# Optimization experiments

Hardware: AMD Instinct MI355X
Metric: run time of the kernel (lower is better)

The kernel has to match this reference:

```python
import jax, jax.numpy as jnp
import numpy as np

# Dims: B=batch, S=seq, H=hidden, I=intermediate, E=experts, K=top-k
B, S, H, I, E, K = 1, 1024, 1024, 1024, 8, 2


def setup_inputs() -> dict:
    key = jax.random.key(0)
    k0, k1, k2, k3 = jax.random.split(key, 4)
    return {
        "hidden_states": jax.random.normal(k0, (B, S, H), dtype=jnp.float32),
        "router_weight": jax.random.normal(k1, (E, H), dtype=jnp.float32) * 0.02,
        "gate_up_proj": jax.random.normal(k2, (E, H, 2 * I), dtype=jnp.float32) * 0.02,
        "gate_up_proj_bias": jnp.zeros((E, 2 * I), dtype=jnp.float32),
        "down_proj": jax.random.normal(k3, (E, I, H), dtype=jnp.float32) * 0.02,
        "down_proj_bias": jnp.zeros((E, H), dtype=jnp.float32),
    }


def reference(hidden_states, router_weight, gate_up_proj, gate_up_proj_bias,
              down_proj, down_proj_bias):
    b, s, h = hidden_states.shape
    flat = hidden_states.reshape(b * s, h)            # [N, H]
    n = flat.shape[0]

    # Router: softmax over experts, then top-k selection
    logits = flat @ router_weight.T                   # [N, E]
    scores = jax.nn.softmax(logits, axis=-1)          # [N, E]
    _, indices = jax.lax.top_k(scores, K)             # [N, K]

    # Dense all-experts GEMM (matches original: every token through every expert)
    gate_up = jnp.einsum('nh,eho->neo', flat, gate_up_proj) + gate_up_proj_bias  # [N, E, 2I]
    gate = jnp.minimum(gate_up[..., ::2], 7.0)        # interleaved gate, clamp max
    up = jnp.clip(gate_up[..., 1::2], -7.0, 7.0)      # interleaved up, clamp both
    activated = (up + 1.0) * gate * jax.nn.sigmoid(gate * 1.702)  # [N, E, I]

    expert_out = jnp.einsum('nei,eih->neh', activated, down_proj) + down_proj_bias  # [N, E, H]

    # Masked combine: zero weights except at top-k experts
    top_w = jnp.take_along_axis(scores, indices, axis=-1)                     # [N, K]
    weights = jnp.zeros_like(scores).at[jnp.arange(n)[:, None], indices].set(top_w)  # [N, E]
    out = (expert_out * weights[..., None]).sum(axis=1)                       # [N, H]
    return out.reshape(b, s, h), scores
```

## Files before the change

### kernel.cpp

```cpp
#include <hip/hip_runtime.h>
#include <hip/hip_bf16.h>

typedef __attribute__((ext_vector_type(8))) short short8;
typedef __attribute__((ext_vector_type(4))) float f32x4;

#define NTOK 1024
#define HDIM 1024
#define IDIM 1024
#define NEXP 8
#define NCOL 2048

#define WS_COUNTS   0
#define WS_Q        960
#define WS_LTOK     1024
#define WS_LW       (WS_LTOK + NEXP*NTOK*4)
#define WS_XBF      131072
#define WS_ACT      (WS_XBF + NTOK*HDIM*2)
#define WS_W1B      (WS_ACT + 2*NTOK*IDIM*2)
#define WS_W2B      (WS_W1B + (size_t)NEXP*NCOL*HDIM*2)

static __device__ __forceinline__ unsigned short f2bf(float x) {
    __hip_bfloat16 h = __float2bfloat16(x);
    return __builtin_bit_cast(unsigned short, h);
}

#define GLDS16(g, l) __builtin_amdgcn_global_load_lds( \
    (const __attribute__((address_space(1))) void*)(g), \
    (__attribute__((address_space(3))) void*)(l), 16, 0, 0)

static __device__ __forceinline__ float4 xpose4(float4 v, int i) {
    float x = (i & 1) ? v.x : v.y;
    float y = (i & 1) ? v.z : v.w;
    x = __shfl_xor(x, 1); y = __shfl_xor(y, 1);
    if (i & 1) { v.x = x; v.z = y; } else { v.y = x; v.w = y; }
    float x2 = (i & 2) ? v.x : v.z;
    float y2 = (i & 2) ? v.y : v.w;
    x2 = __shfl_xor(x2, 2); y2 = __shfl_xor(y2, 2);
    if (i & 2) { v.x = x2; v.y = y2; } else { v.z = x2; v.w = y2; }
    return v;
}

__global__ __launch_bounds__(256) void prep_kernel(
    const float* __restrict__ flat, const float* __restrict__ rw,
    const float* __restrict__ gup,
    float* __restrict__ scores, int* __restrict__ counts,
    int* __restrict__ ltok, float* __restrict__ lw,
    unsigned short* __restrict__ xbf, unsigned short* __restrict__ w1b)
{
    __shared__ unsigned short tile[64][70];
    const int b = blockIdx.x;
    const int t = threadIdx.x;

    if (b >= 256) {
        const int tid = b - 256;
        const int e = tid >> 9, rem = tid & 511, kb = rem >> 5, cb = rem & 31;
        const int i4 = t & 3, g = t >> 2;
        const int rq = g >> 4, cq = (g & 15) * 4;
        const float* s0 = gup + ((size_t)e * 1024 + kb * 64 + rq * 16 + i4) * NCOL
                         + cb * 64 + cq;
        float4 vr[4];
#pragma unroll
        for (int it = 0; it < 4; ++it)
            vr[it] = *(const float4*)(s0 + (size_t)(it * 4) * NCOL);
        const int c = cq + i4;
#pragma unroll
        for (int it = 0; it < 4; ++it) {
            float4 v = xpose4(vr[it], i4);
            ushort4 o;
            o.x = f2bf(v.x); o.y = f2bf(v.y); o.z = f2bf(v.z); o.w = f2bf(v.w);
            *(ushort4*)&tile[c][rq * 16 + it * 4] = o;
        }
        __syncthreads();
        unsigned short* d0 = w1b + (((size_t)e * 16 + kb) * NCOL + cb * 64) * 64;
#pragma unroll
        for (int p = 0; p < 2; ++p) {
            int cc = p * 32 + (t >> 3), q = t & 7;
            short8 vv = *(const short8*)&tile[cc][q * 8];
            *(short8*)&d0[(size_t)cc * 64 + q * 8] = vv;
        }
        return;
    }

    const int n = b * 4 + (t >> 6);
    const int l = t & 63;
    float acc[NEXP];
#pragma unroll
    for (int e = 0; e < NEXP; ++e) acc[e] = 0.f;
    const float* xrow = flat + (size_t)n * HDIM;
#pragma unroll
    for (int j = 0; j < 4; ++j) {
        int h = j * 256 + l * 4;
        float4 v = *(const float4*)&xrow[h];
        ushort4 xb;
        xb.x = f2bf(v.x); xb.y = f2bf(v.y); xb.z = f2bf(v.z); xb.w = f2bf(v.w);
        *(ushort4*)&xbf[(size_t)n * HDIM + h] = xb;
#pragma unroll
        for (int e = 0; e < NEXP; ++e) {
            float4 wv = *(const float4*)&rw[e * HDIM + h];
            acc[e] += v.x * wv.x + v.y * wv.y + v.z * wv.z + v.w * wv.w;
        }
    }
#pragma unroll
    for (int e = 0; e < NEXP; ++e) {
#pragma unroll
        for (int off = 32; off > 0; off >>= 1)
            acc[e] += __shfl_down(acc[e], off);
    }
    if (l == 0) {
        float m = acc[0];
#pragma unroll
        for (int e = 1; e < NEXP; ++e) m = fmaxf(m, acc[e]);
        float s = 0.f, p[NEXP];
#pragma unroll
        for (int e = 0; e < NEXP; ++e) { p[e] = __expf(acc[e] - m); s += p[e]; }
        float inv = 1.f / s;
#pragma unroll
        for (int e = 0; e < NEXP; ++e) { p[e] *= inv; scores[n * NEXP + e] = p[e]; }
        int i0 = 0;
#pragma unroll
        for (int e = 1; e < NEXP; ++e) if (p[e] > p[i0]) i0 = e;
        int i1 = (i0 == 0) ? 1 : 0;
#pragma unroll
        for (int e = 0; e < NEXP; ++e) if (e != i0 && p[e] > p[i1]) i1 = e;
        int pos0 = atomicAdd(&counts[i0 * 32], 1);
        ltok[i0 * NTOK + pos0] = n; lw[i0 * NTOK + pos0] = p[i0];
        int pos1 = atomicAdd(&counts[i1 * 32], 1);
        ltok[i1 * NTOK + pos1] = n; lw[i1 * NTOK + pos1] = p[i1];
    }
}

__global__ __launch_bounds__(512) void gemm1_kernel(
    const unsigned short* __restrict__ xbf, const unsigned short* __restrict__ w1b,
    const float* __restrict__ gbias,
    const int* __restrict__ counts,
    const int* __restrict__ ltok, unsigned short* __restrict__ act,
    const float* __restrict__ dp, unsigned short* __restrict__ w2b,
    int* __restrict__ tq)
{
    const int e = blockIdx.z;
    int cnt = 0, off = 0;
#pragma unroll
    for (int j2 = 0; j2 < NEXP; ++j2) {
        int c = counts[j2 * 32];
        if (j2 < e) off += c;
        if (j2 == e) cnt = c;
    }
    const int by = blockIdx.y;
    const int bx = blockIdx.x;
    const int t = threadIdx.x;

    __shared__ unsigned short As[2][128][64];
    __shared__ unsigned short Bs[2][128][64];
    __shared__ int toks[128];
    __shared__ int tbase;

    if (by * 128 >= cnt) {
        unsigned short (*ttile)[64][70] = (unsigned short (*)[64][70])(&As[0][0][0]);
        const int half = t >> 8, tt = t & 255;
        const int i4 = tt & 3, g = tt >> 2;
        const int rq = g >> 4, cq = (g & 15) * 4;
        for (;;) {
            if (t == 0) tbase = atomicAdd(tq, 2);
            __syncthreads();
            int base = tbase;
            if (base >= 2048) break;
            int myt = base + half;
            int te = myt >> 8, rem = myt & 255, kb = rem >> 4, cb = rem & 15;
            const float* s0 = dp + ((size_t)te * 1024 + kb * 64 + rq * 16 + i4) * HDIM
                             + cb * 64 + cq;
            float4 vr[4];
#pragma unroll
            for (int it = 0; it < 4; ++it)
                vr[it] = *(const float4*)(s0 + (size_t)(it * 4) * HDIM);
            const int c = cq + i4;
#pragma unroll
            for (int it = 0; it < 4; ++it) {
                float4 v = xpose4(vr[it], i4);
                ushort4 o;
                o.x = f2bf(v.x); o.y = f2bf(v.y); o.z = f2bf(v.z); o.w = f2bf(v.w);
                *(ushort4*)&ttile[half][c][rq * 16 + it * 4] = o;
            }
            __syncthreads();
            unsigned short* d0 = w2b + (((size_t)te * 16 + kb) * HDIM + cb * 64) * 64;
#pragma unroll
            for (int p = 0; p < 2; ++p) {
                int cc = p * 32 + (tt >> 3), q = tt & 7;
                short8 vv = *(const short8*)&ttile[half][cc][q * 8];
                *(short8*)&d0[(size_t)cc * 64 + q * 8] = vv;
            }
        }
        return;
    }

    const int l = t & 63, w = t >> 6;
    const int wm = w >> 2, wn = w & 3;
    if (t < 128) toks[t] = ltok[e * NTOK + min(by * 128 + t, cnt - 1)];
    __syncthreads();

    const int li = l & 7, lr = l >> 3;
    const int kswz = (li ^ lr) * 8;
    const unsigned short* asrc[2];
    const unsigned short* bsrc[2];
#pragma unroll
    for (int j = 0; j < 2; ++j) {
        int rr = (w * 2 + j) * 8 + lr;
        asrc[j] = xbf + (size_t)toks[rr] * HDIM + kswz;
        bsrc[j] = w1b + (size_t)e * 16 * NCOL * 64 + (size_t)(bx * 128 + rr) * 64 + kswz;
    }

    f32x4 acc[4][2];
#pragma unroll
    for (int m = 0; m < 4; ++m)
#pragma unroll
        for (int n = 0; n < 2; ++n) acc[m][n] = 0.f;

#pragma unroll
    for (int j = 0; j < 2; ++j) {
        GLDS16(asrc[j], &As[0][(w * 2 + j) * 8][0]);
        GLDS16(bsrc[j], &Bs[0][(w * 2 + j) * 8][0]);
    }

    const int lg = l >> 4, lo = l & 15;
    const int cq0 = ((0 + lg) ^ (lo & 7)) * 8;
    const int cq1 = ((4 + lg) ^ (lo & 7)) * 8;

    for (int ks = 0; ks < HDIM / 64; ++ks) {
        const int p = ks & 1;
        __builtin_amdgcn_s_barrier();
        if (ks + 1 < HDIM / 64) {
            const int kadvA = (ks + 1) * 64;
            const size_t kadvB = (size_t)(ks + 1) * NCOL * 64;
#pragma unroll
            for (int j = 0; j < 2; ++j) {
                GLDS16(asrc[j] + kadvA, &As[p ^ 1][(w * 2 + j) * 8][0]);
                GLDS16(bsrc[j] + kadvB, &Bs[p ^ 1][(w * 2 + j) * 8][0]);
            }
            asm volatile("s_waitcnt vmcnt(4)" ::: "memory");
        } else {
            asm volatile("s_waitcnt vmcnt(0)" ::: "memory");
        }
        __builtin_amdgcn_sched_barrier(0);
        __builtin_amdgcn_s_barrier();
#pragma unroll
        for (int q = 0; q < 2; ++q) {
            const int cq = q ? cq1 : cq0;
            short8 a0 = *(const short8*)&As[p][wm * 64 +  0 + lo][cq];
            short8 a1 = *(const short8*)&As[p][wm * 64 + 16 + lo][cq];
            short8 a2 = *(const short8*)&As[p][wm * 64 + 32 + lo][cq];
            short8 a3 = *(const short8*)&As[p][wm * 64 + 48 + lo][cq];
            short8 b0 = *(const short8*)&Bs[p][wn * 32 +  0 + lo][cq];
            short8 b1 = *(const short8*)&Bs[p][wn * 32 + 16 + lo][cq];
#pragma unroll
            for (int m = 0; m < 4; ++m) {
                short8 am = (m == 0) ? a0 : (m == 1) ? a1 : (m == 2) ? a2 : a3;
                acc[m][0] = __builtin_amdgcn_mfma_f32_16x16x32_bf16(am, b0, acc[m][0], 0, 0, 0);
                acc[m][1] = __builtin_amdgcn_mfma_f32_16x16x32_bf16(am, b1, acc[m][1], 0, 0, 0);
            }
        }
    }

    const int rj = lg * 4;
#pragma unroll
    for (int m = 0; m < 4; ++m) {
#pragma unroll
        for (int n = 0; n < 2; ++n) {
            int col = bx * 128 + wn * 32 + n * 16 + lo;
            float bias = gbias[e * NCOL + col];
#pragma unroll
            for (int j = 0; j < 4; ++j) {
                int slot = by * 128 + wm * 64 + m * 16 + rj + j;
                float val = acc[m][n][j] + bias;
                float other = __shfl_xor(val, 1);
                float g = (l & 1) ? other : val;
                float u = (l & 1) ? val : other;
                g = fminf(g, 7.f);
                u = fminf(fmaxf(u, -7.f), 7.f);
                float av = (u + 1.f) * g * (1.f / (1.f + __expf(-1.702f * g)));
                if (!(l & 1) && slot < cnt)
                    act[(size_t)(off + slot) * IDIM + (col >> 1)] = f2bf(av);
            }
        }
    }
}

__global__ __launch_bounds__(512) void gemm2_kernel(
    const unsigned short* __restrict__ act, const unsigned short* __restrict__ w2b,
    const float* __restrict__ dbias,
    const int* __restrict__ counts,
    const int* __restrict__ ltok,
    const float* __restrict__ lw, float* __restrict__ outbuf)
{
    const int e = blockIdx.z;
    int cnt = 0, off = 0;
#pragma unroll
    for (int j2 = 0; j2 < NEXP; ++j2) {
        int c = counts[j2 * 32];
        if (j2 < e) off += c;
        if (j2 == e) cnt = c;
    }
    const int by = blockIdx.y;
    if (by * 128 >= cnt) return;
    const int bx = blockIdx.x;
    const int t = threadIdx.x;
    const int l = t & 63, w = t >> 6;
    const int wm = w >> 1, wn = w & 1;

    __shared__ unsigned short As[2][128][64];
    __shared__ unsigned short Bs[2][64][64];
    __shared__ int toks[128];
    __shared__ float wts[128];
    if (t < 128) {
        int cl = min(by * 128 + t, cnt - 1);
        toks[t] = ltok[e * NTOK + cl];
        wts[t]  = lw[e * NTOK + cl];
    }
    __syncthreads();

    const int li = l & 7, lr = l >> 3;
    const int kswz = (li ^ lr) * 8;
    const unsigned short* asrc[2];
#pragma unroll
    for (int j = 0; j < 2; ++j) {
        int rr = (w * 2 + j) * 8 + lr;
        asrc[j] = act + (size_t)(off + min(by * 128 + rr, cnt - 1)) * IDIM + kswz;
    }
    const unsigned short* bsrc = w2b + (size_t)e * 16 * HDIM * 64
                               + (size_t)(bx * 64 + w * 8 + lr) * 64 + kswz;

    f32x4 acc[2][2];
#pragma unroll
    for (int m = 0; m < 2; ++m)
#pragma unroll
        for (int n = 0; n < 2; ++n) acc[m][n] = 0.f;

#pragma unroll
    for (int j = 0; j < 2; ++j)
        GLDS16(asrc[j], &As[0][(w * 2 + j) * 8][0]);
    GLDS16(bsrc, &Bs[0][w * 8][0]);

    const int lg = l >> 4, lo = l & 15;
    const int cq0 = ((0 + lg) ^ (lo & 7)) * 8;
    const int cq1 = ((4 + lg) ^ (lo & 7)) * 8;

    for (int ks = 0; ks < IDIM / 64; ++ks) {
        const int p = ks & 1;
        __builtin_amdgcn_s_barrier();
        if (ks + 1 < IDIM / 64) {
            const int kadvA = (ks + 1) * 64;
            const size_t kadvB = (size_t)(ks + 1) * HDIM * 64;
#pragma unroll
            for (int j = 0; j < 2; ++j)
                GLDS16(asrc[j] + kadvA, &As[p ^ 1][(w * 2 + j) * 8][0]);
            GLDS16(bsrc + kadvB, &Bs[p ^ 1][w * 8][0]);
            asm volatile("s_waitcnt vmcnt(3)" ::: "memory");
        } else {
            asm volatile("s_waitcnt vmcnt(0)" ::: "memory");
        }
        __builtin_amdgcn_sched_barrier(0);
        __builtin_amdgcn_s_barrier();
#pragma unroll
        for (int q = 0; q < 2; ++q) {
            const int cq = q ? cq1 : cq0;
            short8 a0 = *(const short8*)&As[p][wm * 32 +  0 + lo][cq];
            short8 a1 = *(const short8*)&As[p][wm * 32 + 16 + lo][cq];
            short8 b0 = *(const short8*)&Bs[p][wn * 32 +  0 + lo][cq];
            short8 b1 = *(const short8*)&Bs[p][wn * 32 + 16 + lo][cq];
            acc[0][0] = __builtin_amdgcn_mfma_f32_16x16x32_bf16(a0, b0, acc[0][0], 0, 0, 0);
            acc[1][0] = __builtin_amdgcn_mfma_f32_16x16x32_bf16(a1, b0, acc[1][0], 0, 0, 0);
            acc[0][1] = __builtin_amdgcn_mfma_f32_16x16x32_bf16(a0, b1, acc[0][1], 0, 0, 0);
            acc[1][1] = __builtin_amdgcn_mfma_f32_16x16x32_bf16(a1, b1, acc[1][1], 0, 0, 0);
        }
    }

    const int rj = lg * 4;
#pragma unroll
    for (int m = 0; m < 2; ++m) {
#pragma unroll
        for (int n = 0; n < 2; ++n) {
            int col = bx * 64 + wn * 32 + n * 16 + lo;
            float bias = dbias[e * HDIM + col];
#pragma unroll
            for (int j = 0; j < 4; ++j) {
                int sl = wm * 32 + m * 16 + rj + j;
                int slot = by * 128 + sl;
                if (slot < cnt) {
                    float val = (acc[m][n][j] + bias) * wts[sl];
                    atomicAdd(&outbuf[(size_t)toks[sl] * HDIM + col], val);
                }
            }
        }
    }
}

extern "C" void kernel_launch(void* const* d_in, const int* in_sizes, int n_in,
                              void* d_out, int out_size, void* d_ws, size_t ws_size,
                              hipStream_t stream) {
    const float* flat  = (const float*)d_in[0];
    const float* rw    = (const float*)d_in[1];
    const float* gup   = (const float*)d_in[2];
    const float* gbias = (const float*)d_in[3];
    const float* dp    = (const float*)d_in[4];
    const float* dbias = (const float*)d_in[5];
    float* out    = (float*)d_out;
    float* scores = out + (size_t)NTOK * HDIM;

    char* ws = (char*)d_ws;
    int*   counts  = (int*)(ws + WS_COUNTS);
    int*   tq      = (int*)(ws + WS_Q);
    int*   ltok    = (int*)(ws + WS_LTOK);
    float* lw      = (float*)(ws + WS_LW);
    unsigned short* xbf = (unsigned short*)(ws + WS_XBF);
    unsigned short* act = (unsigned short*)(ws + WS_ACT);
    unsigned short* w1b = (unsigned short*)(ws + WS_W1B);
    unsigned short* w2b = (unsigned short*)(ws + WS_W2B);

    hipMemsetAsync(ws, 0, 1024, stream);
    hipMemsetAsync(out, 0, (size_t)NTOK * HDIM * sizeof(float), stream);
    prep_kernel<<<4352, 256, 0, stream>>>(flat, rw, gup, scores, counts,
                                          ltok, lw, xbf, w1b);
    gemm1_kernel<<<dim3(16, 8, NEXP), 512, 0, stream>>>(xbf, w1b, gbias, counts,
                                                        ltok, act, dp, w2b, tq);
    gemm2_kernel<<<dim3(16, 8, NEXP), 512, 0, stream>>>(act, w2b, dbias, counts,
                                                        ltok, lw, out);
}
```

Before: 92.37 us.

## Halve GEMM K-tile to 32 and enlarge gemm2 output tile to 128x128

```diff
diff --git a/kernel.cpp b/kernel.cpp
--- a/kernel.cpp
+++ b/kernel.cpp
@@ -55,14 +55,14 @@
         const int tid = b - 256;
         const int e = tid >> 9, rem = tid & 511, kb = rem >> 5, cb = rem & 31;
         const int i4 = t & 3, g = t >> 2;
-        const int rq = g >> 4, cq = (g & 15) * 4;
+        const int rq = g >> 4, cq4 = (g & 15) * 4;
         const float* s0 = gup + ((size_t)e * 1024 + kb * 64 + rq * 16 + i4) * NCOL
-                         + cb * 64 + cq;
+                         + cb * 64 + cq4;
         float4 vr[4];
 #pragma unroll
         for (int it = 0; it < 4; ++it)
             vr[it] = *(const float4*)(s0 + (size_t)(it * 4) * NCOL);
-        const int c = cq + i4;
+        const int c = cq4 + i4;
 #pragma unroll
         for (int it = 0; it < 4; ++it) {
             float4 v = xpose4(vr[it], i4);
@@ -71,12 +71,12 @@
             *(ushort4*)&tile[c][rq * 16 + it * 4] = o;
         }
         __syncthreads();
-        unsigned short* d0 = w1b + (((size_t)e * 16 + kb) * NCOL + cb * 64) * 64;
+        unsigned short* d0 = w1b + (((size_t)e * 32 + kb * 2) * NCOL + cb * 64) * 32;
 #pragma unroll
         for (int p = 0; p < 2; ++p) {
             int cc = p * 32 + (t >> 3), q = t & 7;
             short8 vv = *(const short8*)&tile[cc][q * 8];
-            *(short8*)&d0[(size_t)cc * 64 + q * 8] = vv;
+            *(short8*)&d0[(size_t)(q >> 2) * NCOL * 32 + (size_t)cc * 32 + (q & 3) * 8] = vv;
         }
         return;
     }
@@ -137,6 +137,10 @@
     const float* __restrict__ dp, unsigned short* __restrict__ w2b,
     int* __restrict__ tq)
 {
+    extern __shared__ unsigned short dyn[];
+    __shared__ int toks[128];
+    __shared__ int tbase;
+
     const int e = blockIdx.z;
     int cnt = 0, off = 0;
 #pragma unroll
@@ -145,20 +149,13 @@
         if (j2 < e) off += c;
         if (j2 == e) cnt = c;
     }
-    const int by = blockIdx.y;
-    const int bx = blockIdx.x;
+    const int by = blockIdx.y, bx = blockIdx.x;
     const int t = threadIdx.x;
 
-    __shared__ unsigned short As[2][128][64];
-    __shared__ unsigned short Bs[2][128][64];
-    __shared__ int toks[128];
-    __shared__ int tbase;
-
     if (by * 128 >= cnt) {
-        unsigned short (*ttile)[64][70] = (unsigned short (*)[64][70])(&As[0][0][0]);
         const int half = t >> 8, tt = t & 255;
         const int i4 = tt & 3, g = tt >> 2;
-        const int rq = g >> 4, cq = (g & 15) * 4;
+        const int rq = g >> 4, cq4 = (g & 15) * 4;
         for (;;) {
             if (t == 0) tbase = atomicAdd(tq, 2);
             __syncthreads();
@@ -167,26 +164,26 @@
             int myt = base + half;
             int te = myt >> 8, rem = myt & 255, kb = rem >> 4, cb = rem & 15;
             const float* s0 = dp + ((size_t)te * 1024 + kb * 64 + rq * 16 + i4) * HDIM
-                             + cb * 64 + cq;
+                             + cb * 64 + cq4;
             float4 vr[4];
 #pragma unroll
             for (int it = 0; it < 4; ++it)
                 vr[it] = *(const float4*)(s0 + (size_t)(it * 4) * HDIM);
-            const int c = cq + i4;
+            const int c = cq4 + i4;
 #pragma unroll
             for (int it = 0; it < 4; ++it) {
                 float4 v = xpose4(vr[it], i4);
                 ushort4 o;
                 o.x = f2bf(v.x); o.y = f2bf(v.y); o.z = f2bf(v.z); o.w = f2bf(v.w);
-                *(ushort4*)&ttile[half][c][rq * 16 + it * 4] = o;
+                *(ushort4*)&dyn[half * 4480 + c * 70 + rq * 16 + it * 4] = o;
             }
             __syncthreads();
-            unsigned short* d0 = w2b + (((size_t)te * 16 + kb) * HDIM + cb * 64) * 64;
+            unsigned short* d0 = w2b + (((size_t)te * 32 + kb * 2) * HDIM + cb * 64) * 32;
 #pragma unroll
             for (int p = 0; p < 2; ++p) {
                 int cc = p * 32 + (tt >> 3), q = tt & 7;
-                short8 vv = *(const short8*)&ttile[half][cc][q * 8];
-                *(short8*)&d0[(size_t)cc * 64 + q * 8] = vv;
+                short8 vv = *(const short8*)&dyn[half * 4480 + cc * 70 + q * 8];
+                *(short8*)&d0[(size_t)(q >> 2) * HDIM * 32 + (size_t)cc * 32 + (q & 3) * 8] = vv;
             }
         }
         return;
@@ -197,16 +194,11 @@
     if (t < 128) toks[t] = ltok[e * NTOK + min(by * 128 + t, cnt - 1)];
     __syncthreads();
 
-    const int li = l & 7, lr = l >> 3;
-    const int kswz = (li ^ lr) * 8;
-    const unsigned short* asrc[2];
-    const unsigned short* bsrc[2];
-#pragma unroll
-    for (int j = 0; j < 2; ++j) {
-        int rr = (w * 2 + j) * 8 + lr;
-        asrc[j] = xbf + (size_t)toks[rr] * HDIM + kswz;
-        bsrc[j] = w1b + (size_t)e * 16 * NCOL * 64 + (size_t)(bx * 128 + rr) * 64 + kswz;
-    }
+    const int lr4 = l >> 2, li4 = l & 3;
+    const int fsw = (li4 ^ (lr4 & 3) ^ ((lr4 >> 2) & 3)) * 8;
+    const unsigned short* asrc = xbf + (size_t)toks[w * 16 + lr4] * HDIM + fsw;
+    const unsigned short* bsrc = w1b + (size_t)e * 32 * NCOL * 32
+                               + (size_t)(bx * 128 + w * 16 + lr4) * 32 + fsw;
 
     f32x4 acc[4][2];
 #pragma unroll
@@ -214,48 +206,37 @@
 #pragma unroll
         for (int n = 0; n < 2; ++n) acc[m][n] = 0.f;
 
-#pragma unroll
-    for (int j = 0; j < 2; ++j) {
-        GLDS16(asrc[j], &As[0][(w * 2 + j) * 8][0]);
-        GLDS16(bsrc[j], &Bs[0][(w * 2 + j) * 8][0]);
-    }
+    GLDS16(asrc, dyn + w * 512);
+    GLDS16(bsrc, dyn + 8192 + w * 512);
 
     const int lg = l >> 4, lo = l & 15;
-    const int cq0 = ((0 + lg) ^ (lo & 7)) * 8;
-    const int cq1 = ((4 + lg) ^ (lo & 7)) * 8;
-
-    for (int ks = 0; ks < HDIM / 64; ++ks) {
+    const int cq = (lg ^ (lo & 3) ^ ((lo >> 2) & 3)) * 8;
+
+    for (int ks = 0; ks < 32; ++ks) {
         const int p = ks & 1;
         __builtin_amdgcn_s_barrier();
-        if (ks + 1 < HDIM / 64) {
-            const int kadvA = (ks + 1) * 64;
-            const size_t kadvB = (size_t)(ks + 1) * NCOL * 64;
-#pragma unroll
-            for (int j = 0; j < 2; ++j) {
-                GLDS16(asrc[j] + kadvA, &As[p ^ 1][(w * 2 + j) * 8][0]);
-                GLDS16(bsrc[j] + kadvB, &Bs[p ^ 1][(w * 2 + j) * 8][0]);
-            }
-            asm volatile("s_waitcnt vmcnt(4)" ::: "memory");
+        if (ks + 1 < 32) {
+            GLDS16(asrc + (ks + 1) * 32, dyn + (p ^ 1) * 4096 + w * 512);
+            GLDS16(bsrc + (size_t)(ks + 1) * NCOL * 32, dyn + 8192 + (p ^ 1) * 4096 + w * 512);
+            asm volatile("s_waitcnt vmcnt(2)" ::: "memory");
         } else {
             asm volatile("s_waitcnt vmcnt(0)" ::: "memory");
         }
         __builtin_amdgcn_sched_barrier(0);
         __builtin_amdgcn_s_barrier();
-#pragma unroll
-        for (int q = 0; q < 2; ++q) {
-            const int cq = q ? cq1 : cq0;
-            short8 a0 = *(const short8*)&As[p][wm * 64 +  0 + lo][cq];
-            short8 a1 = *(const short8*)&As[p][wm * 64 + 16 + lo][cq];
-            short8 a2 = *(const short8*)&As[p][wm * 64 + 32 + lo][cq];
-            short8 a3 = *(const short8*)&As[p][wm * 64 + 48 + lo][cq];
-            short8 b0 = *(const short8*)&Bs[p][wn * 32 +  0 + lo][cq];
-            short8 b1 = *(const short8*)&Bs[p][wn * 32 + 16 + lo][cq];
-#pragma unroll
-            for (int m = 0; m < 4; ++m) {
-                short8 am = (m == 0) ? a0 : (m == 1) ? a1 : (m == 2) ? a2 : a3;
-                acc[m][0] = __builtin_amdgcn_mfma_f32_16x16x32_bf16(am, b0, acc[m][0], 0, 0, 0);
-                acc[m][1] = __builtin_amdgcn_mfma_f32_16x16x32_bf16(am, b1, acc[m][1], 0, 0, 0);
-            }
+        const unsigned short* Ap = dyn + p * 4096;
+        const unsigned short* Bp = dyn + 8192 + p * 4096;
+        short8 a0 = *(const short8*)(Ap + (wm * 64 +  0 + lo) * 32 + cq);
+        short8 a1 = *(const short8*)(Ap + (wm * 64 + 16 + lo) * 32 + cq);
+        short8 a2 = *(const short8*)(Ap + (wm * 64 + 32 + lo) * 32 + cq);
+        short8 a3 = *(const short8*)(Ap + (wm * 64 + 48 + lo) * 32 + cq);
+        short8 b0 = *(const short8*)(Bp + (wn * 32 +  0 + lo) * 32 + cq);
+        short8 b1 = *(const short8*)(Bp + (wn * 32 + 16 + lo) * 32 + cq);
+#pragma unroll
+        for (int m = 0; m < 4; ++m) {
+            short8 am = (m == 0) ? a0 : (m == 1) ? a1 : (m == 2) ? a2 : a3;
+            acc[m][0] = __builtin_amdgcn_mfma_f32_16x16x32_bf16(am, b0, acc[m][0], 0, 0, 0);
+            acc[m][1] = __builtin_amdgcn_mfma_f32_16x16x32_bf16(am, b1, acc[m][1], 0, 0, 0);
         }
     }
 
@@ -303,10 +284,10 @@
     const int bx = blockIdx.x;
     const int t = threadIdx.x;
     const int l = t & 63, w = t >> 6;
-    const int wm = w >> 1, wn = w & 1;
-
-    __shared__ unsigned short As[2][128][64];
-    __shared__ unsigned short Bs[2][64][64];
+    const int wm = w >> 2, wn = w & 3;
+
+    __shared__ unsigned short As[2][128][32];
+    __shared__ unsigned short Bs[2][128][32];
     __shared__ int toks[128];
     __shared__ float wts[128];
     if (t < 128) {
@@ -316,72 +297,61 @@
     }
     __syncthreads();
 
-    const int li = l & 7, lr = l >> 3;
-    const int kswz = (li ^ lr) * 8;
-    const unsigned short* asrc[2];
-#pragma unroll
-    for (int j = 0; j < 2; ++j) {
-        int rr = (w * 2 + j) * 8 + lr;
-        asrc[j] = act + (size_t)(off + min(by * 128 + rr, cnt - 1)) * IDIM + kswz;
-    }
-    const unsigned short* bsrc = w2b + (size_t)e * 16 * HDIM * 64
-                               + (size_t)(bx * 64 + w * 8 + lr) * 64 + kswz;
-
-    f32x4 acc[2][2];
-#pragma unroll
-    for (int m = 0; m < 2; ++m)
+    const int lr4 = l >> 2, li4 = l & 3;
+    const int fsw = (li4 ^ (lr4 & 3) ^ ((lr4 >> 2) & 3)) * 8;
+    const unsigned short* asrc = act
+        + (size_t)(off + min(by * 128 + w * 16 + lr4, cnt - 1)) * IDIM + fsw;
+    const unsigned short* bsrc = w2b + (size_t)e * 32 * HDIM * 32
+                               + (size_t)(bx * 128 + w * 16 + lr4) * 32 + fsw;
+
+    f32x4 acc[4][2];
+#pragma unroll
+    for (int m = 0; m < 4; ++m)
 #pragma unroll
         for (int n = 0; n < 2; ++n) acc[m][n] = 0.f;
 
-#pragma unroll
-    for (int j = 0; j < 2; ++j)
-        GLDS16(asrc[j], &As[0][(w * 2 + j) * 8][0]);
-    GLDS16(bsrc, &Bs[0][w * 8][0]);
+    GLDS16(asrc, &As[0][w * 16][0]);
+    GLDS16(bsrc, &Bs[0][w * 16][0]);
 
     const int lg = l >> 4, lo = l & 15;
-    const int cq0 = ((0 + lg) ^ (lo & 7)) * 8;
-    const int cq1 = ((4 + lg) ^ (lo & 7)) * 8;
-
-    for (int ks = 0; ks < IDIM / 64; ++ks) {
+    const int cq = (lg ^ (lo & 3) ^ ((lo >> 2) & 3)) * 8;
+
+    for (int ks = 0; ks < 32; ++ks) {
         const int p = ks & 1;
         __builtin_amdgcn_s_barrier();
-        if (ks + 1 < IDIM / 64) {
-            const int kadvA = (ks + 1) * 64;
-            const size_t kadvB = (size_t)(ks + 1) * HDIM * 64;
-#pragma unroll
-            for (int j = 0; j < 2; ++j)
-                GLDS16(asrc[j] + kadvA, &As[p ^ 1][(w * 2 + j) * 8][0]);
-            GLDS16(bsrc + kadvB, &Bs[p ^ 1][w * 8][0]);
-            asm volatile("s_waitcnt vmcnt(3)" ::: "memory");
+        if (ks + 1 < 32) {
+            GLDS16(asrc + (ks + 1) * 32, &As[p ^ 1][w * 16][0]);
+            GLDS16(bsrc + (size_t)(ks + 1) * HDIM * 32, &Bs[p ^ 1][w * 16][0]);
+            asm volatile("s_waitcnt vmcnt(2)" ::: "memory");
         } else {
             asm volatile("s_waitcnt vmcnt(0)" ::: "memory");
         }
         __builtin_amdgcn_sched_barrier(0);
         __builtin_amdgcn_s_barrier();
-#pragma unroll
-        for (int q = 0; q < 2; ++q) {
-            const int cq = q ? cq1 : cq0;
-            short8 a0 = *(const short8*)&As[p][wm * 32 +  0 + lo][cq];
-            short8 a1 = *(const short8*)&As[p][wm * 32 + 16 + lo][cq];
-            short8 b0 = *(const short8*)&Bs[p][wn * 32 +  0 + lo][cq];
-            short8 b1 = *(const short8*)&Bs[p][wn * 32 + 16 + lo][cq];
-            acc[0][0] = __builtin_amdgcn_mfma_f32_16x16x32_bf16(a0, b0, acc[0][0], 0, 0, 0);
-            acc[1][0] = __builtin_amdgcn_mfma_f32_16x16x32_bf16(a1, b0, acc[1][0], 0, 0, 0);
-            acc[0][1] = __builtin_amdgcn_mfma_f32_16x16x32_bf16(a0, b1, acc[0][1], 0, 0, 0);
-            acc[1][1] = __builtin_amdgcn_mfma_f32_16x16x32_bf16(a1, b1, acc[1][1], 0, 0, 0);
+        short8 a0 = *(const short8*)&As[p][wm * 64 +  0 + lo][cq];
+        short8 a1 = *(const short8*)&As[p][wm * 64 + 16 + lo][cq];
+        short8 a2 = *(const short8*)&As[p][wm * 64 + 32 + lo][cq];
+        short8 a3 = *(const short8*)&As[p][wm * 64 + 48 + lo][cq];
+        short8 b0 = *(const short8*)&Bs[p][wn * 32 +  0 + lo][cq];
+        short8 b1 = *(const short8*)&Bs[p][wn * 32 + 16 + lo][cq];
+#pragma unroll
+        for (int m = 0; m < 4; ++m) {
+            short8 am = (m == 0) ? a0 : (m == 1) ? a1 : (m == 2) ? a2 : a3;
+            acc[m][0] = __builtin_amdgcn_mfma_f32_16x16x32_bf16(am, b0, acc[m][0], 0, 0, 0);
+            acc[m][1] = __builtin_amdgcn_mfma_f32_16x16x32_bf16(am, b1, acc[m][1], 0, 0, 0);
         }
     }
 
     const int rj = lg * 4;
 #pragma unroll
-    for (int m = 0; m < 2; ++m) {
+    for (int m = 0; m < 4; ++m) {
 #pragma unroll
         for (int n = 0; n < 2; ++n) {
-            int col = bx * 64 + wn * 32 + n * 16 + lo;
+            int col = bx * 128 + wn * 32 + n * 16 + lo;
             float bias = dbias[e * HDIM + col];
 #pragma unroll
             for (int j = 0; j < 4; ++j) {
-                int sl = wm * 32 + m * 16 + rj + j;
+                int sl = wm * 64 + m * 16 + rj + j;
                 int slot = by * 128 + sl;
                 if (slot < cnt) {
                     float val = (acc[m][n][j] + bias) * wts[sl];
@@ -418,8 +388,8 @@
     hipMemsetAsync(out, 0, (size_t)NTOK * HDIM * sizeof(float), stream);
     prep_kernel<<<4352, 256, 0, stream>>>(flat, rw, gup, scores, counts,
                                           ltok, lw, xbf, w1b);
-    gemm1_kernel<<<dim3(16, 8, NEXP), 512, 0, stream>>>(xbf, w1b, gbias, counts,
-                                                        ltok, act, dp, w2b, tq);
-    gemm2_kernel<<<dim3(16, 8, NEXP), 512, 0, stream>>>(act, w2b, dbias, counts,
-                                                        ltok, lw, out);
-}
+    gemm1_kernel<<<dim3(16, 8, NEXP), 512, 32768, stream>>>(xbf, w1b, gbias, counts,
+                                                            ltok, act, dp, w2b, tq);
+    gemm2_kernel<<<dim3(8, 8, NEXP), 512, 0, stream>>>(act, w2b, dbias, counts,
+                                                       ltok, lw, out);
+}
```

New measurement: 244.5 us. +164.7%, slower.
